# Performance work log

Measured on AMD Instinct MI355X. Metric: run time of the kernel, lower is better.

Reference implementation:

```python
import jax, jax.numpy as jnp
import numpy as np
from jax import lax

IOU_THRESHOLD = 0.1
B, N = 4, 8192


def setup_inputs() -> dict:
    key = jax.random.key(0)
    # [B, 5, N]: rows 0..3 = cx, cy, w, h; row 4 = confidence score in (0, 1)
    outputs = jax.random.uniform(key, (B, 5, N), dtype=jnp.float32)
    return {"outputs": outputs}


def _nms_single(p):
    """Greedy NMS on one image. p: [5, N] -> [5, N] with kept boxes
    compacted to the front (original column order preserved) and the rest
    zero-padded. Matches the torch loop: repeatedly take the highest-scoring
    surviving box, drop all boxes with IoU >= threshold (box keeps itself),
    and drop boxes with score <= 0."""
    boxes, scores = p[:4], p[4]
    n = scores.shape[0]
    order = jnp.argsort(-scores)            # descending score order
    b = boxes[:, order]

    x1 = b[0] - b[2] * 0.5
    y1 = b[1] - b[3] * 0.5
    x2 = b[0] + b[2] * 0.5
    y2 = b[1] + b[3] * 0.5
    area = (x2 - x1) * (y2 - y1)

    iw = jnp.clip(jnp.minimum(x2[:, None], x2[None, :]) - jnp.maximum(x1[:, None], x1[None, :]), 0.0)
    ih = jnp.clip(jnp.minimum(y2[:, None], y2[None, :]) - jnp.maximum(y1[:, None], y1[None, :]), 0.0)
    inter = iw * ih
    union = area[:, None] + area[None, :] - inter
    iou = inter / (union + 1e-8)            # [N, N] in sorted order

    idx_range = jnp.arange(n)
    keep_init = scores[order] > 0           # non_zero_scores filter

    def body(i, keep):
        # if box i (in score order) survives, suppress j with IoU >= thr, j != i
        row_keep = (iou[i] < IOU_THRESHOLD) | (idx_range == i)
        return jnp.where(keep[i], keep & row_keep, keep)

    keep_sorted = lax.fori_loop(0, n, body, keep_init)

    # map keep mask back to original column order
    keep_orig = jnp.zeros((n,), bool).at[order].set(keep_sorted)
    # stable compaction: kept columns first, original relative order preserved
    perm = jnp.argsort(jnp.where(keep_orig, 0, 1), stable=True)
    gathered = p[:, perm]                    # [5, N]
    valid = idx_range < jnp.sum(keep_orig)
    return jnp.where(valid[None, :], gathered, 0.0)


def reference(outputs):
    # torch version pads to the max detections across the batch; here we keep
    # the fixed width N (extra columns are zero), same kept values/order.
    return jax.vmap(_nms_single)(outputs)


if __name__ == "__main__":
    inp = setup_inputs()
    out = jax.jit(reference)(**inp)
    print(out.shape, out.dtype)
```

## Files before the change

kernel.cpp:

```cpp
#include <hip/hip_runtime.h>

#pragma clang fp contract(off)

#define NBOX 8192
#define BLK  1024
#define EPT  8
#define NBUCK 4096
#define NB 256
#define IOU_THR 0.1f

typedef unsigned short u16;
typedef unsigned int u32;
typedef unsigned long long u64;

#define MND 0x1.999999p-4

#define SMEM_TOT 161408

__global__ __launch_bounds__(BLK, 4) void nms_kernel(const float* __restrict__ in,
                                                     float* __restrict__ out) {
    __shared__ __align__(16) char smem[SMEM_TOT];
    const int img = blockIdx.x;
    const float* __restrict__ p = in + (size_t)img * 5 * NBOX;
    float* __restrict__ o = out + (size_t)img * 5 * NBOX;
    const int t = threadIdx.x;
    const int lane = t & 63;
    const int wid = t >> 6;

    float4* box   = (float4*)smem;
    u16* A        = (u16*)(smem + 131072);
    float4* bx    = (float4*)(smem + 147456);
    u64 (*mat)[4] = (u64(*)[4])(smem + 151552);
    float4* kx    = (float4*)(smem + 155648);
    u32* pfxA     = (u32*)(smem + 151552);
    u32* kom      = (u32*)(smem + 159744);
    int* wcnt     = (int*)(smem + 160768);
    u64* keptQ    = (u64*)(smem + 160832);
    int* S0sh     = (int*)(smem + 160864);
    u64* skey  = (u64*)smem;
    u32* hist  = (u32*)(smem + 65536);
    u32* bbase = (u32*)(smem + 81920);

    {
        float4 z; z.x = z.y = z.z = z.w = 0.0f;
        float4* o4 = (float4*)o;
#pragma unroll
        for (int e = 0; e < 10; e++) o4[t + e * BLK] = z;
    }

    for (int i = t; i < NBUCK; i += BLK) hist[i] = 0;
    if (t < 256) kom[t] = 0;
    if (t == 0) *S0sh = 0;
    __syncthreads();

    u32 mybkt[EPT], myarr[EPT], mykeyhi[EPT];
#pragma unroll
    for (int e = 0; e < EPT; e++) {
        int j = t + e * BLK;
        float s = p[4 * NBOX + j];
        u32 u = __float_as_uint(s);
        u32 ordb = u ^ (u32)(((int)u >> 31) | (int)0x80000000);
        mykeyhi[e] = ~ordb;
        int vb = (int)(s * (float)NBUCK);
        vb = vb < 0 ? 0 : (vb > NBUCK - 1 ? NBUCK - 1 : vb);
        mybkt[e] = (u32)(NBUCK - 1 - vb);
        myarr[e] = atomicAdd(&hist[mybkt[e]], 1u);
        u64 bal = __ballot(s > 0.0f);
        if (lane == 0) atomicAdd(S0sh, (int)__popcll(bal));
    }
    __syncthreads();

    {
        u32 h0 = hist[4 * t], h1 = hist[4 * t + 1], h2 = hist[4 * t + 2], h3 = hist[4 * t + 3];
        int v = (int)(h0 + h1 + h2 + h3);
        int x = v;
        for (int d = 1; d < 64; d <<= 1) {
            int y = __shfl_up(x, d, 64);
            if (lane >= d) x += y;
        }
        if (lane == 63) wcnt[wid] = x;
        __syncthreads();
        int wb = 0;
        for (int i = 0; i < wid; i++) wb += wcnt[i];
        int excl = wb + x - v;
        bbase[4 * t]     = (u32)excl;
        bbase[4 * t + 1] = (u32)excl + h0;
        bbase[4 * t + 2] = (u32)excl + h0 + h1;
        bbase[4 * t + 3] = (u32)excl + h0 + h1 + h2;
    }
    __syncthreads();

#pragma unroll
    for (int e = 0; e < EPT; e++) {
        u32 pos = bbase[mybkt[e]] + myarr[e];
        skey[pos] = ((u64)mykeyhi[e] << 32) | (u32)(t + e * BLK);
    }
    __syncthreads();

#pragma unroll
    for (int e = 0; e < EPT; e++) {
        u32 b = mybkt[e];
        u32 lo = bbase[b], hi2 = lo + hist[b];
        u64 me = ((u64)mykeyhi[e] << 32) | (u32)(t + e * BLK);
        u32 r = lo;
        for (u32 q = lo; q < hi2; q++) r += (skey[q] < me) ? 1u : 0u;
        A[r] = (u16)(t + e * BLK);
    }
    __syncthreads();
    int S = *S0sh;

#pragma unroll
    for (int e = 0; e < EPT; e++) {
        int j = t + e * BLK;
        float cx = p[j], cy = p[NBOX + j];
        float w_ = p[2 * NBOX + j], h_ = p[3 * NBOX + j];
        box[j] = make_float4(cx - w_ * 0.5f, cy - h_ * 0.5f,
                             cx + w_ * 0.5f, cy + h_ * 0.5f);
    }
    __syncthreads();

    if (t < NB) bx[t] = box[A[t]];
    ((u64*)mat)[t] = 0;
    __syncthreads();

    while (S > 0) {
        int nb = S < NB ? S : NB;

        {
            int i = t >> 2, q = t & 3;
            if (i > 0 && i < nb) {
                int clo = (i * q) >> 2;
                int chi = (i * (q + 1)) >> 2;
                if (chi > clo) {
                    float4 bi = bx[i];
                    float ari = (bi.z - bi.x) * (bi.w - bi.y);
                    u64 acc = 0;
                    for (int c = clo; c < chi; c++) {
                        float4 bc = bx[c];
                        float arc = (bc.z - bc.x) * (bc.w - bc.y);
                        float iw = fmaxf(fminf(bi.z, bc.z) - fmaxf(bi.x, bc.x), 0.0f);
                        float ih = fmaxf(fminf(bi.w, bc.w) - fmaxf(bi.y, bc.y), 0.0f);
                        float inter = iw * ih;
                        float t2 = (ari + arc) - inter;
                        float uu = t2 + 1e-8f;
                        if ((double)inter > MND * (double)uu) acc |= (1ull << (c - clo));
                    }
                    if (acc) {
                        int w0 = clo >> 6, sh = clo & 63;
                        atomicOr(&mat[i][w0], acc << sh);
                        if (sh && (((chi - 1) >> 6) != w0))
                            atomicOr(&mat[i][w0 + 1], acc >> (64 - sh));
                    }
                }
            }
        }
        __syncthreads();

        int tailN = S - nb;
        int C1 = 0, base0 = nb;
        if (tailN > 0) {
            int lim = tailN < 7680 ? tailN : 7680;
            C1 = (lim + 959) / 960;
            base0 = nb + 960 * C1;
        }
        float4 eb[EPT]; float ea[EPT]; u16 ei[EPT];
        u32 am = 0;
        if (wid == 0) {
            u64 r0[4], r1[4], r2[4], r3[4];
#pragma unroll
            for (int wq = 0; wq < 4; wq++) {
                r0[wq] = mat[lane][wq];
                r1[wq] = mat[64 + lane][wq];
                r2[wq] = mat[128 + lane][wq];
                r3[wq] = mat[192 + lane][wq];
            }
            u64 A0, A1, A2, A3;
            {
                int n0 = nb;       A0 = n0 <= 0 ? 0ull : (n0 >= 64 ? ~0ull : ((1ull << n0) - 1ull));
                int n1 = nb - 64;  A1 = n1 <= 0 ? 0ull : (n1 >= 64 ? ~0ull : ((1ull << n1) - 1ull));
                int n2 = nb - 128; A2 = n2 <= 0 ? 0ull : (n2 >= 64 ? ~0ull : ((1ull << n2) - 1ull));
                int n3 = nb - 192; A3 = n3 <= 0 ? 0ull : (n3 >= 64 ? ~0ull : ((1ull << n3) - 1ull));
            }
            u64 K0 = 0, K1 = 0, K2 = 0, K3 = 0;
            u64 lm = (1ull << lane) - 1ull;
            while (A0 | A1 | A2 | A3) {
                bool c0b = ((A0 >> lane) & 1) && !(r0[0] & A0 & lm);
                bool c1b = ((A1 >> lane) & 1) && !((r1[0] & A0) | (r1[1] & A1 & lm));
                bool c2b = ((A2 >> lane) & 1) && !((r2[0] & A0) | (r2[1] & A1) | (r2[2] & A2 & lm));
                bool c3b = ((A3 >> lane) & 1) && !((r3[0] & A0) | (r3[1] & A1) | (r3[2] & A2) | (r3[3] & A3 & lm));
                u64 C0_ = __ballot(c0b), C1_ = __ballot(c1b), C2_ = __ballot(c2b), C3_ = __ballot(c3b);
                K0 |= C0_; K1 |= C1_; K2 |= C2_; K3 |= C3_;
                A0 &= ~C0_; A1 &= ~C1_; A2 &= ~C2_; A3 &= ~C3_;
                bool s0b = ((A0 >> lane) & 1) && ((r0[0] & C0_) | (r0[1] & C1_) | (r0[2] & C2_) | (r0[3] & C3_));
                bool s1b = ((A1 >> lane) & 1) && ((r1[0] & C0_) | (r1[1] & C1_) | (r1[2] & C2_) | (r1[3] & C3_));
                bool s2b = ((A2 >> lane) & 1) && ((r2[0] & C0_) | (r2[1] & C1_) | (r2[2] & C2_) | (r2[3] & C3_));
                bool s3b = ((A3 >> lane) & 1) && ((r3[0] & C0_) | (r3[1] & C1_) | (r3[2] & C2_) | (r3[3] & C3_));
                A0 &= ~__ballot(s0b); A1 &= ~__ballot(s1b); A2 &= ~__ballot(s2b); A3 &= ~__ballot(s3b);
            }
            if (lane < 4) keptQ[lane] = lane == 0 ? K0 : lane == 1 ? K1 : lane == 2 ? K2 : K3;
            {
                int pkb1 = (int)__popcll(K0);
                int pkb2 = pkb1 + (int)__popcll(K1);
                int pkb3 = pkb2 + (int)__popcll(K2);
#pragma unroll
                for (int wq = 0; wq < 4; wq++) {
                    u64 kq = wq == 0 ? K0 : wq == 1 ? K1 : wq == 2 ? K2 : K3;
                    if ((kq >> lane) & 1) {
                        int slot = wq * 64 + lane;
                        int j = (int)A[slot];
                        atomicOr(&kom[j >> 5], 1u << (j & 31));
                        int pk = (wq == 0 ? 0 : wq == 1 ? pkb1 : wq == 2 ? pkb2 : pkb3)
                                 + (int)__popcll(kq & lm);
                        kx[pk] = bx[slot];
                    }
                }
            }
            if (base0 < S) {
                int C0 = (S - base0 + 63) >> 6;
                int st0 = base0 + lane * C0;
#pragma unroll
                for (int e = 0; e < EPT; e++) {
                    int pos = st0 + e;
                    if (e < C0 && pos < S) {
                        u16 j = A[pos];
                        ei[e] = j;
                        float4 b = box[j];
                        eb[e] = b;
                        ea[e] = (b.z - b.x) * (b.w - b.y);
                        am |= (1u << e);
                    }
                }
            }
        } else {
            int ti = t - 64;
            int st = nb + ti * C1;
#pragma unroll
            for (int e = 0; e < EPT; e++) {
                int pos = st + e;
                if (e < C1 && pos < S) {
                    u16 j = A[pos];
                    ei[e] = j;
                    float4 b = box[j];
                    eb[e] = b;
                    ea[e] = (b.z - b.x) * (b.w - b.y);
                    am |= (1u << e);
                }
            }
        }
        __syncthreads();

        if (t < 512) ((u64*)mat)[t] = 0;
        u64 kq0 = keptQ[0], kq1 = keptQ[1], kq2 = keptQ[2], kq3 = keptQ[3];
        int nk = (int)(__popcll(kq0) + __popcll(kq1) + __popcll(kq2) + __popcll(kq3));

        if (am) {
            for (int c = 0; c < nk; c++) {
                float4 cb = kx[c];
                float arc = (cb.z - cb.x) * (cb.w - cb.y);
#pragma unroll
                for (int e = 0; e < EPT; e++) {
                    if (am & (1u << e)) {
                        float iw = fminf(eb[e].z, cb.z) - fmaxf(eb[e].x, cb.x);
                        float ih = fminf(eb[e].w, cb.w) - fmaxf(eb[e].y, cb.y);
                        if (iw > 0.0f && ih > 0.0f) {
                            float inter = iw * ih;
                            float t2 = (ea[e] + arc) - inter;
                            float uu = t2 + 1e-8f;
                            if ((double)inter > MND * (double)uu) am &= ~(1u << e);
                        }
                    }
                }
                if (!am) break;
            }
        }

        {
            int cnt = __popc(am);
            int x = cnt;
            for (int d = 1; d < 64; d <<= 1) {
                int y = __shfl_up(x, d, 64);
                if (lane >= d) x += y;
            }
            if (lane == 63) wcnt[wid] = x;
            __syncthreads();
            int wb = 0, tot = 0;
            for (int i = 0; i < 16; i++) tot += wcnt[i];
            if (wid == 0) {
                for (int i = 1; i < 16; i++) wb += wcnt[i];
            } else {
                for (int i = 1; i < wid; i++) wb += wcnt[i];
            }
            int off = wb + x - cnt;
#pragma unroll
            for (int e = 0; e < EPT; e++) {
                if (am & (1u << e)) {
                    A[off] = ei[e];
                    if (off < NB) bx[off] = eb[e];
                    off++;
                }
            }
            if (t >= 512) ((u64*)mat)[t] = 0;
            __syncthreads();
            S = tot;
        }
    }
    __syncthreads();

    {
        u32 w = (t < 256) ? kom[t] : 0u;
        int c = __popc(w);
        int x = c;
        for (int d = 1; d < 64; d <<= 1) {
            int y = __shfl_up(x, d, 64);
            if (lane >= d) x += y;
        }
        if (lane == 63) wcnt[wid] = x;
        __syncthreads();
        int wb = 0;
        for (int i = 0; i < wid; i++) wb += wcnt[i];
        if (t < 256) pfxA[t] = (u32)(wb + x - c);
    }
    __syncthreads();
    for (int j = t; j < NBOX; j += BLK) {
        u32 km = kom[j >> 5];
        if ((km >> (j & 31)) & 1u) {
            int pos = (int)(pfxA[j >> 5] + (u32)__popc(km & ((1u << (j & 31)) - 1u)));
            o[0 * NBOX + pos] = p[0 * NBOX + j];
            o[1 * NBOX + pos] = p[1 * NBOX + j];
            o[2 * NBOX + pos] = p[2 * NBOX + j];
            o[3 * NBOX + pos] = p[3 * NBOX + j];
            o[4 * NBOX + pos] = p[4 * NBOX + j];
        }
    }
}

extern "C" void kernel_launch(void* const* d_in, const int* in_sizes, int n_in,
                              void* d_out, int out_size, void* d_ws, size_t ws_size,
                              hipStream_t stream) {
    const float* in = (const float*)d_in[0];
    float* out = (float*)d_out;
    int B = in_sizes[0] / (5 * NBOX);
    hipLaunchKernelGGL(nms_kernel, dim3(B), dim3(BLK), 0, stream, in, out);
}
```

Measured before the change: 152.2 us.

## Keep surviving boxes in thread registers instead of compacting into shared arrays

Each thread now holds a fixed block of sorted boxes in registers for the whole NMS loop. Each round a prefix count picks the next 256-box leader block, instead of rewriting a compacted index array and reloading boxes from shared memory after every round. Kept-box areas are precomputed into a shared array, and the kept-index bitmap is updated by the owning threads. This cuts shared memory use and per-round gather traffic, but every thread keeps iterating its full register slice, which makes work per thread less balanced as the survivors thin out.

```diff
diff --git a/kernel.cpp b/kernel.cpp
--- a/kernel.cpp
+++ b/kernel.cpp
@@ -7,7 +7,6 @@
 #define EPT  8
 #define NBUCK 4096
 #define NB 256
-#define IOU_THR 0.1f
 
 typedef unsigned short u16;
 typedef unsigned int u32;
@@ -15,7 +14,7 @@
 
 #define MND 0x1.999999p-4
 
-#define SMEM_TOT 161408
+#define SMEM_TOT 148736
 
 __global__ __launch_bounds__(BLK, 4) void nms_kernel(const float* __restrict__ in,
                                                      float* __restrict__ out) {
@@ -27,19 +26,20 @@
     const int lane = t & 63;
     const int wid = t >> 6;
 
-    float4* box   = (float4*)smem;
-    u16* A        = (u16*)(smem + 131072);
-    float4* bx    = (float4*)(smem + 147456);
-    u64 (*mat)[4] = (u64(*)[4])(smem + 151552);
-    float4* kx    = (float4*)(smem + 155648);
-    u32* pfxA     = (u32*)(smem + 151552);
-    u32* kom      = (u32*)(smem + 159744);
-    int* wcnt     = (int*)(smem + 160768);
-    u64* keptQ    = (u64*)(smem + 160832);
-    int* S0sh     = (int*)(smem + 160864);
     u64* skey  = (u64*)smem;
     u32* hist  = (u32*)(smem + 65536);
     u32* bbase = (u32*)(smem + 81920);
+    float4* box = (float4*)smem;
+    float4* bx  = (float4*)smem;
+    float* ka   = (float*)(smem + 4608);
+    float4* kx  = (float4*)(smem + 5632);
+    u64 (*mat)[4] = (u64(*)[4])(smem + 9728);
+    u32* pfxA   = (u32*)(smem + 17920);
+    u16* sidx  = (u16*)(smem + 131072);
+    u32* kom   = (u32*)(smem + 147456);
+    int* wcnt  = (int*)(smem + 148480);
+    u64* keptQ = (u64*)(smem + 148544);
+    int* S0sh  = (int*)(smem + 148576);
 
     {
         float4 z; z.x = z.y = z.z = z.w = 0.0f;
@@ -104,10 +104,10 @@
         u64 me = ((u64)mykeyhi[e] << 32) | (u32)(t + e * BLK);
         u32 r = lo;
         for (u32 q = lo; q < hi2; q++) r += (skey[q] < me) ? 1u : 0u;
-        A[r] = (u16)(t + e * BLK);
-    }
-    __syncthreads();
-    int S = *S0sh;
+        sidx[r] = (u16)(t + e * BLK);
+    }
+    __syncthreads();
+    int S0 = *S0sh;
 
 #pragma unroll
     for (int e = 0; e < EPT; e++) {
@@ -119,12 +119,52 @@
     }
     __syncthreads();
 
-    if (t < NB) bx[t] = box[A[t]];
+    float4 eb[EPT]; float ea[EPT];
+    u32 am = 0;
+#pragma unroll
+    for (int e = 0; e < EPT; e++) {
+        int r = t * EPT + e;
+        float4 b = box[sidx[r]];
+        eb[e] = b;
+        ea[e] = (b.z - b.x) * (b.w - b.y);
+        if (r < S0) am |= (1u << e);
+    }
+    __syncthreads();
     ((u64*)mat)[t] = 0;
-    __syncthreads();
-
-    while (S > 0) {
+
+    while (true) {
+        int myAlive = __popc(am);
+        int x = myAlive;
+        for (int d = 1; d < 64; d <<= 1) {
+            int y = __shfl_up(x, d, 64);
+            if (lane >= d) x += y;
+        }
+        if (lane == 63) wcnt[wid] = x;
+        __syncthreads();
+        int wb = 0, S = 0;
+        for (int i = 0; i < 16; i++) {
+            int v = wcnt[i];
+            if (i < wid) wb += v;
+            S += v;
+        }
+        if (S == 0) break;
         int nb = S < NB ? S : NB;
+        int r = wb + x - myAlive;
+
+        u64 spl = 0, sph = 0;
+#pragma unroll
+        for (int e = 0; e < EPT; e++) {
+            if (am & (1u << e)) {
+                if (r < NB) {
+                    bx[r] = eb[e];
+                    u64 v = (u64)(u32)(r + 1) << (16 * (e & 3));
+                    if (e < 4) spl |= v; else sph |= v;
+                    am &= ~(1u << e);
+                }
+                r++;
+            }
+        }
+        __syncthreads();
 
         {
             int i = t >> 2, q = t & 3;
@@ -156,15 +196,6 @@
         }
         __syncthreads();
 
-        int tailN = S - nb;
-        int C1 = 0, base0 = nb;
-        if (tailN > 0) {
-            int lim = tailN < 7680 ? tailN : 7680;
-            C1 = (lim + 959) / 960;
-            base0 = nb + 960 * C1;
-        }
-        float4 eb[EPT]; float ea[EPT]; u16 ei[EPT];
-        u32 am = 0;
         if (wid == 0) {
             u64 r0[4], r1[4], r2[4], r3[4];
 #pragma unroll
@@ -198,65 +229,40 @@
                 A0 &= ~__ballot(s0b); A1 &= ~__ballot(s1b); A2 &= ~__ballot(s2b); A3 &= ~__ballot(s3b);
             }
             if (lane < 4) keptQ[lane] = lane == 0 ? K0 : lane == 1 ? K1 : lane == 2 ? K2 : K3;
-            {
-                int pkb1 = (int)__popcll(K0);
-                int pkb2 = pkb1 + (int)__popcll(K1);
-                int pkb3 = pkb2 + (int)__popcll(K2);
-#pragma unroll
-                for (int wq = 0; wq < 4; wq++) {
-                    u64 kq = wq == 0 ? K0 : wq == 1 ? K1 : wq == 2 ? K2 : K3;
-                    if ((kq >> lane) & 1) {
-                        int slot = wq * 64 + lane;
-                        int j = (int)A[slot];
-                        atomicOr(&kom[j >> 5], 1u << (j & 31));
+        }
+        __syncthreads();
+
+        u64 kq0 = keptQ[0], kq1 = keptQ[1], kq2 = keptQ[2], kq3 = keptQ[3];
+        int nk = (int)(__popcll(kq0) + __popcll(kq1) + __popcll(kq2) + __popcll(kq3));
+        {
+            int pkb1 = (int)__popcll(kq0);
+            int pkb2 = pkb1 + (int)__popcll(kq1);
+            int pkb3 = pkb2 + (int)__popcll(kq2);
+#pragma unroll
+            for (int e = 0; e < EPT; e++) {
+                int se = (int)(((e < 4 ? spl : sph) >> (16 * (e & 3))) & 0xFFFF);
+                if (se) {
+                    int slot = se - 1;
+                    int wq = slot >> 6;
+                    u64 kq = wq == 0 ? kq0 : wq == 1 ? kq1 : wq == 2 ? kq2 : kq3;
+                    if ((kq >> (slot & 63)) & 1) {
+                        int oi = (int)sidx[t * EPT + e];
+                        atomicOr(&kom[oi >> 5], 1u << (oi & 31));
                         int pk = (wq == 0 ? 0 : wq == 1 ? pkb1 : wq == 2 ? pkb2 : pkb3)
-                                 + (int)__popcll(kq & lm);
-                        kx[pk] = bx[slot];
+                                 + (int)__popcll(kq & ((1ull << (slot & 63)) - 1ull));
+                        kx[pk] = eb[e];
+                        ka[pk] = ea[e];
                     }
                 }
             }
-            if (base0 < S) {
-                int C0 = (S - base0 + 63) >> 6;
-                int st0 = base0 + lane * C0;
-#pragma unroll
-                for (int e = 0; e < EPT; e++) {
-                    int pos = st0 + e;
-                    if (e < C0 && pos < S) {
-                        u16 j = A[pos];
-                        ei[e] = j;
-                        float4 b = box[j];
-                        eb[e] = b;
-                        ea[e] = (b.z - b.x) * (b.w - b.y);
-                        am |= (1u << e);
-                    }
-                }
-            }
-        } else {
-            int ti = t - 64;
-            int st = nb + ti * C1;
-#pragma unroll
-            for (int e = 0; e < EPT; e++) {
-                int pos = st + e;
-                if (e < C1 && pos < S) {
-                    u16 j = A[pos];
-                    ei[e] = j;
-                    float4 b = box[j];
-                    eb[e] = b;
-                    ea[e] = (b.z - b.x) * (b.w - b.y);
-                    am |= (1u << e);
-                }
-            }
-        }
-        __syncthreads();
-
-        if (t < 512) ((u64*)mat)[t] = 0;
-        u64 kq0 = keptQ[0], kq1 = keptQ[1], kq2 = keptQ[2], kq3 = keptQ[3];
-        int nk = (int)(__popcll(kq0) + __popcll(kq1) + __popcll(kq2) + __popcll(kq3));
+        }
+        ((u64*)mat)[t] = 0;
+        __syncthreads();
 
         if (am) {
             for (int c = 0; c < nk; c++) {
                 float4 cb = kx[c];
-                float arc = (cb.z - cb.x) * (cb.w - cb.y);
+                float arc = ka[c];
 #pragma unroll
                 for (int e = 0; e < EPT; e++) {
                     if (am & (1u << e)) {
@@ -273,36 +279,6 @@
                 if (!am) break;
             }
         }
-
-        {
-            int cnt = __popc(am);
-            int x = cnt;
-            for (int d = 1; d < 64; d <<= 1) {
-                int y = __shfl_up(x, d, 64);
-                if (lane >= d) x += y;
-            }
-            if (lane == 63) wcnt[wid] = x;
-            __syncthreads();
-            int wb = 0, tot = 0;
-            for (int i = 0; i < 16; i++) tot += wcnt[i];
-            if (wid == 0) {
-                for (int i = 1; i < 16; i++) wb += wcnt[i];
-            } else {
-                for (int i = 1; i < wid; i++) wb += wcnt[i];
-            }
-            int off = wb + x - cnt;
-#pragma unroll
-            for (int e = 0; e < EPT; e++) {
-                if (am & (1u << e)) {
-                    A[off] = ei[e];
-                    if (off < NB) bx[off] = eb[e];
-                    off++;
-                }
-            }
-            if (t >= 512) ((u64*)mat)[t] = 0;
-            __syncthreads();
-            S = tot;
-        }
     }
     __syncthreads();
 
```

Measured after the change: 225.8 us. 48.3% more time.
